# Performance work log

Hardware: AMD Instinct MI355X
Metric: run time of the kernel (lower is better)

Reference implementation:

```python
import jax, jax.numpy as jnp
import numpy as np

L = 4          # layers
HID = 64       # hidden channels per layer
CIN = 16       # patched input channels (1 * 4 * 4)
K = 5
PAD = 2
T_IN, T_OUT = 10, 10
FORGET_BIAS = 1.0
LN_EPS = 1e-5


def _conv(x, w, pad):
    return jax.lax.conv_general_dilated(
        x, w, window_strides=(1, 1), padding=[(pad, pad), (pad, pad)],
        dimension_numbers=('NCHW', 'OIHW', 'NCHW'))


def _ln(x):
    # LayerNorm over (C,H,W) per sample, no affine (gamma=1, beta=0)
    mu = jnp.mean(x, axis=(1, 2, 3), keepdims=True)
    var = jnp.var(x, axis=(1, 2, 3), keepdims=True)
    return (x - mu) * jax.lax.rsqrt(var + LN_EPS)


def _cell(x, h, c, m, Wx, Wh, Wm, Wo, Wl):
    # ST-LSTM cell (PredRNN V1) with layer norm on gate convs
    xcat = _ln(_conv(x, Wx, PAD))   # [B, 7*HID, H, W]
    hcat = _ln(_conv(h, Wh, PAD))   # [B, 4*HID, H, W]
    mcat = _ln(_conv(m, Wm, PAD))   # [B, 3*HID, H, W]
    ix, fx, gx, ixp, fxp, gxp, ox = jnp.split(xcat, 7, axis=1)
    ih, fh, gh, oh = jnp.split(hcat, 4, axis=1)
    im, fm, gm = jnp.split(mcat, 3, axis=1)
    i = jax.nn.sigmoid(ix + ih)
    f = jax.nn.sigmoid(fx + fh + FORGET_BIAS)
    g = jnp.tanh(gx + gh)
    c_new = f * c + i * g
    ip = jax.nn.sigmoid(ixp + im)
    fp = jax.nn.sigmoid(fxp + fm + FORGET_BIAS)
    gp = jnp.tanh(gxp + gm)
    m_new = fp * m + ip * gp
    mem = jnp.concatenate([c_new, m_new], axis=1)  # [B, 2*HID, H, W]
    o = jax.nn.sigmoid(ox + oh + _ln(_conv(mem, Wo, PAD)))
    h_new = o * jnp.tanh(_conv(mem, Wl, 0))        # conv_last is 1x1
    return h_new, c_new, m_new


def _run_layers(x_t, hs, cs, m, Wx0, Wxr, Wh, Wm, Wo, Wl):
    h_list, c_list = [], []
    h0, c0, m = _cell(x_t, hs[0], cs[0], m, Wx0, Wh[0], Wm[0], Wo[0], Wl[0])
    h_list.append(h0); c_list.append(c0)
    for i in range(1, L):
        hi, ci, m = _cell(h_list[-1], hs[i], cs[i], m,
                          Wxr[i - 1], Wh[i], Wm[i], Wo[i], Wl[i])
        h_list.append(hi); c_list.append(ci)
    return jnp.stack(h_list), jnp.stack(c_list), m


def setup_inputs() -> dict:
    key = jax.random.key(0)
    ks = jax.random.split(key, 9)
    s = 0.02
    return {
        'x_patched': jax.random.normal(ks[0], (4, T_IN + T_OUT, CIN, 32, 32), jnp.float32),
        'mask_patched': jax.random.uniform(ks[1], (4, T_IN + T_OUT - 2, 1, 32, 32), jnp.float32),
        'Wx0': jax.random.normal(ks[2], (7 * HID, CIN, K, K), jnp.float32) * s,
        'Wxr': jax.random.normal(ks[3], (L - 1, 7 * HID, HID, K, K), jnp.float32) * s,
        'Wh': jax.random.normal(ks[4], (L, 4 * HID, HID, K, K), jnp.float32) * s,
        'Wm': jax.random.normal(ks[5], (L, 3 * HID, HID, K, K), jnp.float32) * s,
        'Wo': jax.random.normal(ks[6], (L, HID, 2 * HID, K, K), jnp.float32) * s,
        'Wl': jax.random.normal(ks[7], (L, HID, 2 * HID, 1, 1), jnp.float32) * s,
        'Wout': jax.random.normal(ks[8], (CIN, HID, 1, 1), jnp.float32) * s,
    }


def reference(x_patched, mask_patched, Wx0, Wxr, Wh, Wm, Wo, Wl, Wout):
    B, T, _, H, W = x_patched.shape
    hs = jnp.zeros((L, B, HID, H, W), x_patched.dtype)
    cs = jnp.zeros((L, B, HID, H, W), x_patched.dtype)
    m = jnp.zeros((B, HID, H, W), x_patched.dtype)

    # t = 0: reverse scheduled sampling feeds ground truth
    hs, cs, m = _run_layers(x_patched[:, 0], hs, cs, m, Wx0, Wxr, Wh, Wm, Wo, Wl)
    x_out0 = _conv(hs[-1], Wout, 0)

    def scan_fn(carry, inp):
        hs, cs, m, x_out = carry
        x_frame, mask_t = inp
        x_t = mask_t * x_frame + (1.0 - mask_t) * x_out
        hs, cs, m = _run_layers(x_t, hs, cs, m, Wx0, Wxr, Wh, Wm, Wo, Wl)
        x_new = _conv(hs[-1], Wout, 0)
        return (hs, cs, m, x_new), x_new

    # t = 1 .. T-2: mask index t-1
    xs = (jnp.moveaxis(x_patched[:, 1:T - 1], 1, 0),
          jnp.moveaxis(mask_patched[:, :T - 2], 1, 0))
    _, outs = jax.lax.scan(scan_fn, (hs, cs, m, x_out0), xs)  # [T-2, B, CIN, H, W]
    x_next = jnp.concatenate([x_out0[:, None], jnp.moveaxis(outs, 0, 1)], axis=1)
    return x_next  # [B, T-1, CIN, H, W]; decouple_loss is identically 0 for V1
```

## Files before the change

kernel.cpp:

```cpp
#include <hip/hip_runtime.h>
#include <cstddef>
#include <cstdint>


#define BB 4
#define NLAYER 4
#define NSTEP 19

typedef _Float16 f16;
typedef _Float16 f16x8 __attribute__((ext_vector_type(8)));
typedef float f32x4 __attribute__((ext_vector_type(4)));

constexpr size_t OFF_HS    = 0;
constexpr size_t OFF_CS    = 1048576;
constexpr size_t OFF_M     = 2097152;
constexpr size_t OFF_STATS = 2359296;
constexpr size_t OFF_XRAW  = 2359360;
constexpr size_t OFF_HRAW  = 4194368;
constexpr size_t OFF_MRAW  = 5242944;
constexpr size_t OFF_MEM   = 6029376;
constexpr size_t OFF_OPART = 6553664;
constexpr size_t OFF_ORAW  = 7602240;
constexpr size_t OFF_OXH   = 7864384;
constexpr size_t OFF_WF    = 8126528;
constexpr size_t ZERO_N    = OFF_XRAW;

constexpr size_t WF_X0 = 0;
constexpr size_t WF_XR = 716800;
constexpr size_t WF_H  = 5017600;
constexpr size_t WF_M  = 8294400;
constexpr size_t WF_O  = 10752000;

__device__ __forceinline__ float sigmoidf_(float x) {
    return 1.0f / (1.0f + __expf(-x));
}

__device__ __forceinline__ float fast_tanh(float x) {
    float ax = fabsf(x);
    float e = __expf(2.0f * ax);
    float r = 1.0f - 2.0f / (e + 1.0f);
    return copysignf(r, x);
}

__device__ __forceinline__ void ln_params(const double* stats, int slot, int b,
                                          float N, float& mu, float& rs) {
    double s1 = stats[slot * 8 + b * 2 + 0];
    double s2 = stats[slot * 8 + b * 2 + 1];
    double mud = s1 / (double)N;
    double var = s2 / (double)N - mud * mud;
    mu = (float)mud;
    float v = (float)var + 1e-5f;
    float r = rsqrtf(v);
    r = r * (1.5f - 0.5f * v * r * r);
    rs = r;
}

__global__ __launch_bounds__(256)
void prep_k(const float* __restrict__ src, f16* __restrict__ dst,
            int CO, int CIs, int CIp) {
    int idx = blockIdx.x * 256 + threadIdx.x;
    int total = CO * CIp * 25;
    if (idx >= total) return;
    int ci = idx % CIp;
    int rem = idx / CIp;
    int co = rem % CO;
    int tap = rem / CO;
    float v = (ci < CIs) ? src[((size_t)co * CIs + ci) * 25 + tap] : 0.f;
    f16 hi = (f16)v;
    f16 lo = (f16)(v - (float)hi);
    dst[((size_t)(tap * 2 + 0) * CO + co) * CIp + ci] = hi;
    dst[((size_t)(tap * 2 + 1) * CO + co) * CIp + ci] = lo;
}

__global__ __launch_bounds__(256)
void mfconv_k(const float* __restrict__ xsrc, int xbstride, int xCI, int xCIpad,
              const f16* __restrict__ wfx,
              const float* __restrict__ hsrc, const f16* __restrict__ wfh,
              const float* __restrict__ msrc, const f16* __restrict__ wfm,
              const float* __restrict__ x_patched, const float* __restrict__ mask,
              const float* __restrict__ prevout, int t, int domix,
              float* __restrict__ xraw, float* __restrict__ hraw,
              float* __restrict__ mraw, double* __restrict__ stats) {
    __shared__ alignas(16) f16 lds[14208];
    const int tid = threadIdx.x;
    int bid = blockIdx.x;
    const int b = bid / 224;
    int g = bid % 224;
    int path, cog, pxg, CO, CI, CIpad;
    const f16* wf;
    const float* in;
    float* outp;
    if (g < 112) {
        path = 0; cog = g >> 4; pxg = g & 15;
        CO = 448; CI = xCI; CIpad = xCIpad; wf = wfx; outp = xraw;
        in = xsrc + (size_t)b * xbstride;
    } else if (g < 176) {
        g -= 112; path = 1; cog = g >> 4; pxg = g & 15;
        CO = 256; CI = 64; CIpad = 64; wf = wfh; outp = hraw;
        in = hsrc + (size_t)b * 65536;
    } else {
        g -= 176; path = 2; cog = g >> 4; pxg = g & 15;
        CO = 192; CI = 64; CIpad = 64; wf = wfm; outp = mraw;
        in = msrc + (size_t)b * 65536;
    }
    const int y0 = pxg * 2;
    const bool mix = (path == 0) && (domix != 0);

    const int ci_l = tid & 31, sr = tid >> 5;
    const int skg = ci_l >> 3, scb = ci_l & 7;
    const int sy = y0 - 2 + sr;
    const bool rowok = (sr < 6) && ((unsigned)sy < 32u);

    const int w = tid >> 6, lane = tid & 63;
    const int coh = w & 1, wr = w >> 1;
    const int n = lane & 15, kq = lane >> 4;
    const size_t wtap = (size_t)2 * CO * CIpad;
    const size_t laneA = (size_t)(cog * 64 + coh * 32 + n) * CIpad + kq * 8;
    const int pbase = (wr + 2) * 37 + 2 + n;

    f32x4 acc[2][2] = {};

    const int nchunks = CIpad >> 5;
    for (int chunk = 0; chunk < nchunks; ++chunk) {
        __syncthreads();
        {
            const int cig = chunk * 32 + ci_l;
            float v[32];
            #pragma unroll
            for (int k = 0; k < 32; ++k) v[k] = 0.f;
            if (rowok && cig < CI) {
                if (mix) {
                    const float* xfr = x_patched + ((size_t)b * 20 + t) * 16384
                                       + (size_t)cig * 1024 + sy * 32;
                    const float* xor_ = prevout
                                       + (((size_t)b * NSTEP + (t - 1)) * 16 + cig) * 1024
                                       + sy * 32;
                    const float* mkr = mask + ((size_t)b * 18 + (t - 1)) * 1024 + sy * 32;
                    #pragma unroll
                    for (int k = 0; k < 8; ++k) {
                        float4 a = *(const float4*)(xfr + k * 4);
                        float4 o = *(const float4*)(xor_ + k * 4);
                        float4 mm = *(const float4*)(mkr + k * 4);
                        v[4 * k + 0] = mm.x * a.x + (1.f - mm.x) * o.x;
                        v[4 * k + 1] = mm.y * a.y + (1.f - mm.y) * o.y;
                        v[4 * k + 2] = mm.z * a.z + (1.f - mm.z) * o.z;
                        v[4 * k + 3] = mm.w * a.w + (1.f - mm.w) * o.w;
                    }
                } else {
                    const float* rp = in + (size_t)cig * 1024 + sy * 32;
                    #pragma unroll
                    for (int k = 0; k < 8; ++k) {
                        float4 q = *(const float4*)(rp + k * 4);
                        v[4 * k + 0] = q.x; v[4 * k + 1] = q.y;
                        v[4 * k + 2] = q.z; v[4 * k + 3] = q.w;
                    }
                }
            }
            if (sr < 6) {
                #define STW(c, val) { int p = sr * 37 + (c);                         \
                    int s_ = skg ^ ((p >> 1) & 3);                                   \
                    int off = p * 32 + (s_ << 3) + scb;                              \
                    f16 hi = (f16)(val); f16 lo = (f16)((val) - (float)hi);          \
                    lds[off] = hi; lds[7104 + off] = lo; }
                STW(0, 0.f); STW(1, 0.f);
                #pragma unroll
                for (int x = 0; x < 32; ++x) STW(x + 2, v[x]);
                STW(34, 0.f); STW(35, 0.f);
                #undef STW
            }
        }
        __syncthreads();
        const f16* wfc = wf + chunk * 32;
        for (int ky = 0; ky < 5; ++ky) {
            const f16* wfk = wfc + (size_t)(ky * 5) * wtap;
            const int pky = pbase + (ky - 2) * 37;
            #pragma unroll
            for (int kx = 0; kx < 5; ++kx) {
                const f16* wA = wfk + (size_t)kx * wtap;
                const f16* wAl = wA + (size_t)CO * CIpad;
                f16x8 a0h = *(const f16x8*)(wA + laneA);
                f16x8 a1h = *(const f16x8*)(wA + laneA + (size_t)16 * CIpad);
                f16x8 a0l = *(const f16x8*)(wAl + laneA);
                f16x8 a1l = *(const f16x8*)(wAl + laneA + (size_t)16 * CIpad);
                #pragma unroll
                for (int pt = 0; pt < 2; ++pt) {
                    int p = pky + (kx - 2) + pt * 16;
                    int off = p * 32 + ((kq ^ ((p >> 1) & 3)) << 3);
                    f16x8 bh = *(const f16x8*)&lds[off];
                    f16x8 bl = *(const f16x8*)&lds[7104 + off];
                    acc[0][pt] = __builtin_amdgcn_mfma_f32_16x16x32_f16(a0h, bh, acc[0][pt], 0, 0, 0);
                    acc[1][pt] = __builtin_amdgcn_mfma_f32_16x16x32_f16(a1h, bh, acc[1][pt], 0, 0, 0);
                    acc[0][pt] = __builtin_amdgcn_mfma_f32_16x16x32_f16(a0l, bh, acc[0][pt], 0, 0, 0);
                    acc[1][pt] = __builtin_amdgcn_mfma_f32_16x16x32_f16(a1l, bh, acc[1][pt], 0, 0, 0);
                    acc[0][pt] = __builtin_amdgcn_mfma_f32_16x16x32_f16(a0h, bl, acc[0][pt], 0, 0, 0);
                    acc[1][pt] = __builtin_amdgcn_mfma_f32_16x16x32_f16(a1h, bl, acc[1][pt], 0, 0, 0);
                }
            }
        }
    }

    float* ob = outp + ((size_t)b * CO + cog * 64 + coh * 32) * 1024 + (y0 + wr) * 32;
    double s1 = 0.0, s2 = 0.0;
    #pragma unroll
    for (int ct = 0; ct < 2; ++ct)
        #pragma unroll
        for (int pt = 0; pt < 2; ++pt)
            #pragma unroll
            for (int j = 0; j < 4; ++j) {
                float vv = acc[ct][pt][j];
                ob[(size_t)(ct * 16 + kq * 4 + j) * 1024 + pt * 16 + n] = vv;
                s1 += vv; s2 += (double)vv * vv;
            }
    __syncthreads();
    double* red = (double*)lds;
    red[tid] = s1; red[256 + tid] = s2;
    __syncthreads();
    for (int s = 128; s > 0; s >>= 1) {
        if (tid < s) { red[tid] += red[tid + s]; red[256 + tid] += red[256 + tid + s]; }
        __syncthreads();
    }
    if (tid == 0) {
        atomicAdd(&stats[path * 8 + b * 2 + 0], red[0]);
        atomicAdd(&stats[path * 8 + b * 2 + 1], red[256]);
    }
}

__global__ __launch_bounds__(256)
void convo_mf_k(const float* __restrict__ mem, const f16* __restrict__ wfo,
                float* __restrict__ opart) {
    __shared__ alignas(16) f16 lds[14208];
    const int tid = threadIdx.x;
    const int bid = blockIdx.x;
    const int chunk = bid & 3;
    const int pxg = (bid >> 2) & 15;
    const int b = bid >> 6;
    const int y0 = pxg * 2;
    const float* in = mem + (size_t)b * 131072;

    const int ci_l = tid & 31, sr = tid >> 5;
    const int skg = ci_l >> 3, scb = ci_l & 7;
    const int sy = y0 - 2 + sr;
    const bool rowok = (sr < 6) && ((unsigned)sy < 32u);

    const int w = tid >> 6, lane = tid & 63;
    const int coh = w & 1, wr = w >> 1;
    const int n = lane & 15, kq = lane >> 4;
    const size_t wtap = (size_t)2 * 64 * 128;
    const size_t laneA = (size_t)(coh * 32 + n) * 128 + chunk * 32 + kq * 8;
    const int pbase = (wr + 2) * 37 + 2 + n;

    f32x4 acc[2][2] = {};

    {
        const int cig = chunk * 32 + ci_l;
        float v[32];
        #pragma unroll
        for (int k = 0; k < 32; ++k) v[k] = 0.f;
        if (rowok) {
            const float* rp = in + (size_t)cig * 1024 + sy * 32;
            #pragma unroll
            for (int k = 0; k < 8; ++k) {
                float4 q = *(const float4*)(rp + k * 4);
                v[4 * k + 0] = q.x; v[4 * k + 1] = q.y;
                v[4 * k + 2] = q.z; v[4 * k + 3] = q.w;
            }
        }
        if (sr < 6) {
            #define STW(c, val) { int p = sr * 37 + (c);                         \
                int s_ = skg ^ ((p >> 1) & 3);                                   \
                int off = p * 32 + (s_ << 3) + scb;                              \
                f16 hi = (f16)(val); f16 lo = (f16)((val) - (float)hi);          \
                lds[off] = hi; lds[7104 + off] = lo; }
            STW(0, 0.f); STW(1, 0.f);
            #pragma unroll
            for (int x = 0; x < 32; ++x) STW(x + 2, v[x]);
            STW(34, 0.f); STW(35, 0.f);
            #undef STW
        }
    }
    __syncthreads();
    for (int ky = 0; ky < 5; ++ky) {
        const f16* wfk = wfo + (size_t)(ky * 5) * wtap;
        const int pky = pbase + (ky - 2) * 37;
        #pragma unroll
        for (int kx = 0; kx < 5; ++kx) {
            const f16* wA = wfk + (size_t)kx * wtap;
            const f16* wAl = wA + (size_t)64 * 128;
            f16x8 a0h = *(const f16x8*)(wA + laneA);
            f16x8 a1h = *(const f16x8*)(wA + laneA + (size_t)16 * 128);
            f16x8 a0l = *(const f16x8*)(wAl + laneA);
            f16x8 a1l = *(const f16x8*)(wAl + laneA + (size_t)16 * 128);
            #pragma unroll
            for (int pt = 0; pt < 2; ++pt) {
                int p = pky + (kx - 2) + pt * 16;
                int off = p * 32 + ((kq ^ ((p >> 1) & 3)) << 3);
                f16x8 bh = *(const f16x8*)&lds[off];
                f16x8 bl = *(const f16x8*)&lds[7104 + off];
                acc[0][pt] = __builtin_amdgcn_mfma_f32_16x16x32_f16(a0h, bh, acc[0][pt], 0, 0, 0);
                acc[1][pt] = __builtin_amdgcn_mfma_f32_16x16x32_f16(a1h, bh, acc[1][pt], 0, 0, 0);
                acc[0][pt] = __builtin_amdgcn_mfma_f32_16x16x32_f16(a0l, bh, acc[0][pt], 0, 0, 0);
                acc[1][pt] = __builtin_amdgcn_mfma_f32_16x16x32_f16(a1l, bh, acc[1][pt], 0, 0, 0);
                acc[0][pt] = __builtin_amdgcn_mfma_f32_16x16x32_f16(a0h, bl, acc[0][pt], 0, 0, 0);
                acc[1][pt] = __builtin_amdgcn_mfma_f32_16x16x32_f16(a1h, bl, acc[1][pt], 0, 0, 0);
            }
        }
    }
    float* ob = opart + (size_t)chunk * 262144
              + ((size_t)b * 64 + coh * 32) * 1024 + (y0 + wr) * 32;
    #pragma unroll
    for (int ct = 0; ct < 2; ++ct)
        #pragma unroll
        for (int pt = 0; pt < 2; ++pt)
            #pragma unroll
            for (int j = 0; j < 4; ++j)
                ob[(size_t)(ct * 16 + kq * 4 + j) * 1024 + pt * 16 + n] = acc[ct][pt][j];
}

#define LD4(dst, p) { float4 _v = *reinterpret_cast<const float4*>(p); \
                      (dst)[0]=_v.x; (dst)[1]=_v.y; (dst)[2]=_v.z; (dst)[3]=_v.w; }
#define ST4(p, src) { *reinterpret_cast<float4*>(p) = \
                      make_float4((src)[0], (src)[1], (src)[2], (src)[3]); }

__global__ __launch_bounds__(256)
void gates_k(const float* __restrict__ xraw, const float* __restrict__ hraw,
             const float* __restrict__ mraw, double* __restrict__ stats,
             float* __restrict__ cs_l, float* __restrict__ m_buf,
             float* __restrict__ mem, float* __restrict__ oxh) {
    int e4 = blockIdx.x * 256 + threadIdx.x;
    if (e4 < 8) stats[24 + e4] = 0.0;
    int b = e4 >> 14;
    int r = (e4 & 16383) << 2;

    float mu_x, rs_x, mu_h, rs_h, mu_m, rs_m;
    ln_params(stats, 0, b, 458752.f, mu_x, rs_x);
    ln_params(stats, 1, b, 262144.f, mu_h, rs_h);
    ln_params(stats, 2, b, 196608.f, mu_m, rs_m);

    const float* xb = xraw + (size_t)b * 458752 + r;
    const float* hb = hraw + (size_t)b * 262144 + r;
    const float* mb = mraw + (size_t)b * 196608 + r;
    float* csb  = cs_l  + (size_t)b * 65536 + r;
    float* mbb  = m_buf + (size_t)b * 65536 + r;
    float* memc = mem   + (size_t)b * 131072 + r;
    float* memm = memc + 65536;
    float* oxb  = oxh   + (size_t)b * 65536 + r;

    float X[7][4], H[4][4], M[3][4], C[4], MM[4];
    #pragma unroll
    for (int k = 0; k < 7; ++k) LD4(X[k], xb + k * 65536);
    #pragma unroll
    for (int k = 0; k < 4; ++k) LD4(H[k], hb + k * 65536);
    #pragma unroll
    for (int k = 0; k < 3; ++k) LD4(M[k], mb + k * 65536);
    LD4(C, csb);
    LD4(MM, mbb);

    float cn[4], mn[4], ox4[4];
    #pragma unroll
    for (int j = 0; j < 4; ++j) {
        float ix  = (X[0][j] - mu_x) * rs_x;
        float fx  = (X[1][j] - mu_x) * rs_x;
        float gx  = (X[2][j] - mu_x) * rs_x;
        float ixp = (X[3][j] - mu_x) * rs_x;
        float fxp = (X[4][j] - mu_x) * rs_x;
        float gxp = (X[5][j] - mu_x) * rs_x;
        float ox  = (X[6][j] - mu_x) * rs_x;
        float ih  = (H[0][j] - mu_h) * rs_h;
        float fh  = (H[1][j] - mu_h) * rs_h;
        float gh  = (H[2][j] - mu_h) * rs_h;
        float oh  = (H[3][j] - mu_h) * rs_h;
        float im  = (M[0][j] - mu_m) * rs_m;
        float fm  = (M[1][j] - mu_m) * rs_m;
        float gm  = (M[2][j] - mu_m) * rs_m;

        float i  = sigmoidf_(ix + ih);
        float f  = sigmoidf_(fx + fh + 1.0f);
        float gg = fast_tanh(gx + gh);
        float c  = f * C[j] + i * gg;
        float ip = sigmoidf_(ixp + im);
        float fp = sigmoidf_(fxp + fm + 1.0f);
        float gp = fast_tanh(gxp + gm);
        float m2 = fp * MM[j] + ip * gp;
        cn[j] = c; mn[j] = m2; ox4[j] = ox + oh;
    }
    ST4(csb, cn); ST4(mbb, mn); ST4(memc, cn); ST4(memm, mn); ST4(oxb, ox4);
}

__global__ __launch_bounds__(256)
void statso_k(const float* __restrict__ opart, float* __restrict__ oraw,
              double* __restrict__ stats) {
    __shared__ double red[512];
    int e4 = blockIdx.x * 256 + threadIdx.x;
    int b = e4 >> 14;
    int r = e4 << 2;
    float4 v0 = *reinterpret_cast<const float4*>(opart + r);
    float4 v1 = *reinterpret_cast<const float4*>(opart + 262144 + r);
    float4 v2 = *reinterpret_cast<const float4*>(opart + 524288 + r);
    float4 v3 = *reinterpret_cast<const float4*>(opart + 786432 + r);
    float4 s;
    s.x = v0.x + v1.x + v2.x + v3.x;
    s.y = v0.y + v1.y + v2.y + v3.y;
    s.z = v0.z + v1.z + v2.z + v3.z;
    s.w = v0.w + v1.w + v2.w + v3.w;
    *reinterpret_cast<float4*>(oraw + r) = s;
    double s1 = (double)s.x + (double)s.y + (double)s.z + (double)s.w;
    double s2 = (double)s.x * s.x + (double)s.y * s.y +
                (double)s.z * s.z + (double)s.w * s.w;
    int t = threadIdx.x;
    red[t] = s1; red[256 + t] = s2;
    __syncthreads();
    for (int st = 128; st > 0; st >>= 1) {
        if (t < st) { red[t] += red[t + st]; red[256 + t] += red[256 + t + st]; }
        __syncthreads();
    }
    if (t == 0) {
        atomicAdd(&stats[24 + b * 2 + 0], red[0]);
        atomicAdd(&stats[24 + b * 2 + 1], red[256]);
    }
}

__global__ __launch_bounds__(256)
void final_k(const float* __restrict__ mem, const float* __restrict__ oraw,
             const float* __restrict__ oxh, double* __restrict__ stats,
             const float* __restrict__ Wl_l, float* __restrict__ hs_l) {
    int bi = blockIdx.x;
    int b = bi >> 4, pxq = (bi >> 2) & 3, coq = bi & 3;
    int px = pxq * 256 + threadIdx.x;
    const float* memb = mem + (size_t)b * 131072 + px;
    float acc[16];
    #pragma unroll
    for (int k = 0; k < 16; ++k) acc[k] = 0.f;
    for (int ci = 0; ci < 128; ++ci) {
        float v = memb[ci * 1024];
        #pragma unroll
        for (int k = 0; k < 16; ++k)
            acc[k] = fmaf(v, Wl_l[(coq * 16 + k) * 128 + ci], acc[k]);
    }
    float mu, rs;
    ln_params(stats, 3, b, 65536.f, mu, rs);
    #pragma unroll
    for (int k = 0; k < 16; ++k) {
        int co = coq * 16 + k;
        size_t idx = ((size_t)b * 64 + co) * 1024 + px;
        float o = sigmoidf_(oxh[idx] + (oraw[idx] - mu) * rs);
        hs_l[idx] = o * fast_tanh(acc[k]);
    }
    if (bi == 0 && threadIdx.x < 24) stats[threadIdx.x] = 0.0;
}

__global__ __launch_bounds__(256)
void out_k(const float* __restrict__ h3, const float* __restrict__ Wout,
           float* __restrict__ out, int t) {
    int e = blockIdx.x * 256 + threadIdx.x;
    int b = e >> 10, px = e & 1023;
    const float* hb = h3 + (size_t)b * 65536 + px;
    float acc[16];
    #pragma unroll
    for (int k = 0; k < 16; ++k) acc[k] = 0.f;
    for (int ci = 0; ci < 64; ++ci) {
        float v = hb[ci * 1024];
        #pragma unroll
        for (int k = 0; k < 16; ++k) acc[k] = fmaf(v, Wout[k * 64 + ci], acc[k]);
    }
    #pragma unroll
    for (int k = 0; k < 16; ++k)
        out[(((size_t)b * NSTEP + t) * 16 + k) * 1024 + px] = acc[k];
}

__global__ __launch_bounds__(256)
void init_k(float* __restrict__ ws) {
    size_t i = ((size_t)blockIdx.x * 256 + threadIdx.x) * 4;
    for (; i < ZERO_N; i += (size_t)gridDim.x * 1024)
        *reinterpret_cast<float4*>(ws + i) = make_float4(0.f, 0.f, 0.f, 0.f);
}

extern "C" void kernel_launch(void* const* d_in, const int* in_sizes, int n_in,
                              void* d_out, int out_size, void* d_ws, size_t ws_size,
                              hipStream_t stream) {
    const float* x_patched = (const float*)d_in[0];
    const float* mask      = (const float*)d_in[1];
    const float* Wx0       = (const float*)d_in[2];
    const float* Wxr       = (const float*)d_in[3];
    const float* Wh        = (const float*)d_in[4];
    const float* Wm        = (const float*)d_in[5];
    const float* Wo        = (const float*)d_in[6];
    const float* Wl        = (const float*)d_in[7];
    const float* Wout      = (const float*)d_in[8];
    float* out = (float*)d_out;
    float* ws  = (float*)d_ws;

    float* hs    = ws + OFF_HS;
    float* cs    = ws + OFF_CS;
    float* m_buf = ws + OFF_M;
    double* stats = (double*)(ws + OFF_STATS);
    float* xraw  = ws + OFF_XRAW;
    float* hraw  = ws + OFF_HRAW;
    float* mraw  = ws + OFF_MRAW;
    float* mem   = ws + OFF_MEM;
    float* opart = ws + OFF_OPART;
    float* oraw  = ws + OFF_ORAW;
    float* oxh   = ws + OFF_OXH;
    f16*   wfb   = (f16*)(ws + OFF_WF);

    init_k<<<1024, 256, 0, stream>>>(ws);

    prep_k<<<(448 * 32 * 25 + 255) / 256, 256, 0, stream>>>(
        Wx0, wfb + WF_X0, 448, 16, 32);
    for (int lr = 0; lr < 3; ++lr)
        prep_k<<<(448 * 64 * 25 + 255) / 256, 256, 0, stream>>>(
            Wxr + (size_t)lr * 448 * 64 * 25, wfb + WF_XR + (size_t)lr * 1433600,
            448, 64, 64);
    for (int l = 0; l < 4; ++l)
        prep_k<<<(256 * 64 * 25 + 255) / 256, 256, 0, stream>>>(
            Wh + (size_t)l * 256 * 64 * 25, wfb + WF_H + (size_t)l * 819200,
            256, 64, 64);
    for (int l = 0; l < 4; ++l)
        prep_k<<<(192 * 64 * 25 + 255) / 256, 256, 0, stream>>>(
            Wm + (size_t)l * 192 * 64 * 25, wfb + WF_M + (size_t)l * 614400,
            192, 64, 64);
    for (int l = 0; l < 4; ++l)
        prep_k<<<(64 * 128 * 25 + 255) / 256, 256, 0, stream>>>(
            Wo + (size_t)l * 64 * 128 * 25, wfb + WF_O + (size_t)l * 409600,
            64, 128, 128);

    for (int t = 0; t < NSTEP; ++t) {
        for (int l = 0; l < NLAYER; ++l) {
            const float* xsrc;
            int xbstride, domix, xCI, xCIpad;
            const f16* wfx;
            if (l == 0) {
                xsrc = x_patched; xCI = 16; xCIpad = 32; wfx = wfb + WF_X0;
                if (t == 0) { xbstride = 327680; domix = 0; }
                else        { xbstride = 0;      domix = 1; }
            } else {
                xsrc = hs + (size_t)(l - 1) * 262144;
                xbstride = 65536; domix = 0; xCI = 64; xCIpad = 64;
                wfx = wfb + WF_XR + (size_t)(l - 1) * 1433600;
            }
            mfconv_k<<<dim3(BB * 224), 256, 0, stream>>>(
                xsrc, xbstride, xCI, xCIpad, wfx,
                hs + (size_t)l * 262144, wfb + WF_H + (size_t)l * 819200,
                m_buf, wfb + WF_M + (size_t)l * 614400,
                x_patched, mask, out, t, domix,
                xraw, hraw, mraw, stats);
            gates_k<<<256, 256, 0, stream>>>(
                xraw, hraw, mraw, stats,
                cs + (size_t)l * 262144, m_buf, mem, oxh);
            convo_mf_k<<<dim3(256), 256, 0, stream>>>(
                mem, wfb + WF_O + (size_t)l * 409600, opart);
            statso_k<<<256, 256, 0, stream>>>(opart, oraw, stats);
            final_k<<<64, 256, 0, stream>>>(
                mem, oraw, oxh, stats,
                Wl + (size_t)l * 64 * 128, hs + (size_t)l * 262144);
        }
        out_k<<<16, 256, 0, stream>>>(hs + 3 * 262144, Wout, out, t);
    }
    (void)in_sizes; (void)n_in; (void)out_size; (void)ws_size;
}
```

Baseline: 13.47 ms.

## Fuse all per-step kernels into one persistent kernel with software grid barriers

Replaces the roughly 400 separate kernel launches (weight prep, conv, gates, conv_o, stats, final, output) with a single persistent kernel of 256 blocks that loops over timesteps and layers and uses an atomic-counter grid barrier between phases. The goal is to remove per-launch overhead and inter-kernel gaps on a latency-bound recurrent workload. The main conv phase now runs 896 work units over 256 blocks, so per-phase parallelism drops compared with the 896-block launches. The separate partial-sum buffer for conv_o is removed, and the persistent design depends on all 256 blocks being co-resident to avoid deadlock.

```diff
diff --git a/kernel.cpp b/kernel.cpp
--- a/kernel.cpp
+++ b/kernel.cpp
@@ -3,9 +3,9 @@
 #include <cstdint>
 
 
-#define BB 4
 #define NLAYER 4
 #define NSTEP 19
+#define GRID 256
 
 typedef _Float16 f16;
 typedef _Float16 f16x8 __attribute__((ext_vector_type(8)));
@@ -19,10 +19,10 @@
 constexpr size_t OFF_HRAW  = 4194368;
 constexpr size_t OFF_MRAW  = 5242944;
 constexpr size_t OFF_MEM   = 6029376;
-constexpr size_t OFF_OPART = 6553664;
-constexpr size_t OFF_ORAW  = 7602240;
-constexpr size_t OFF_OXH   = 7864384;
-constexpr size_t OFF_WF    = 8126528;
+constexpr size_t OFF_ORAW  = 6553664;
+constexpr size_t OFF_OXH   = 6815808;
+constexpr size_t OFF_WF    = 7077952;
+constexpr size_t OFF_BAR   = 13273152;
 constexpr size_t ZERO_N    = OFF_XRAW;
 
 constexpr size_t WF_X0 = 0;
@@ -30,6 +30,19 @@
 constexpr size_t WF_H  = 5017600;
 constexpr size_t WF_M  = 8294400;
 constexpr size_t WF_O  = 10752000;
+
+struct P {
+    const float* x_patched; const float* mask;
+    const float* Wx0; const float* Wxr; const float* Wh;
+    const float* Wm; const float* Wo; const float* Wl; const float* Wout;
+    float* out;
+    float* hs; float* cs; float* m_buf;
+    double* stats;
+    float* xraw; float* hraw; float* mraw;
+    float* mem; float* oraw; float* oxh;
+    f16* wfx0; f16* wfxr; f16* wfh; f16* wfm; f16* wfo;
+    unsigned* bar; unsigned* gen;
+};
 
 __device__ __forceinline__ float sigmoidf_(float x) {
     return 1.0f / (1.0f + __expf(-x));
@@ -55,56 +68,73 @@
     rs = r;
 }
 
-__global__ __launch_bounds__(256)
-void prep_k(const float* __restrict__ src, f16* __restrict__ dst,
-            int CO, int CIs, int CIp) {
-    int idx = blockIdx.x * 256 + threadIdx.x;
+__device__ __forceinline__ void gridbar(unsigned* bar, unsigned* gen) {
+    __syncthreads();
+    if (threadIdx.x == 0) {
+        __threadfence();
+        unsigned g = __hip_atomic_load(gen, __ATOMIC_RELAXED, __HIP_MEMORY_SCOPE_AGENT);
+        unsigned v = __hip_atomic_fetch_add(bar, 1u, __ATOMIC_ACQ_REL, __HIP_MEMORY_SCOPE_AGENT);
+        if (v == (unsigned)GRID - 1u) {
+            __hip_atomic_store(bar, 0u, __ATOMIC_RELAXED, __HIP_MEMORY_SCOPE_AGENT);
+            __hip_atomic_fetch_add(gen, 1u, __ATOMIC_RELEASE, __HIP_MEMORY_SCOPE_AGENT);
+        } else {
+            while (__hip_atomic_load(gen, __ATOMIC_ACQUIRE, __HIP_MEMORY_SCOPE_AGENT) == g)
+                __builtin_amdgcn_s_sleep(8);
+        }
+        __threadfence();
+    }
+    __syncthreads();
+}
+
+__device__ void prep_dev(const float* __restrict__ src, f16* __restrict__ dst,
+                         int CO, int CIs, int CIp, int gid, int gs) {
     int total = CO * CIp * 25;
-    if (idx >= total) return;
-    int ci = idx % CIp;
-    int rem = idx / CIp;
-    int co = rem % CO;
-    int tap = rem / CO;
-    float v = (ci < CIs) ? src[((size_t)co * CIs + ci) * 25 + tap] : 0.f;
-    f16 hi = (f16)v;
-    f16 lo = (f16)(v - (float)hi);
-    dst[((size_t)(tap * 2 + 0) * CO + co) * CIp + ci] = hi;
-    dst[((size_t)(tap * 2 + 1) * CO + co) * CIp + ci] = lo;
-}
-
-__global__ __launch_bounds__(256)
-void mfconv_k(const float* __restrict__ xsrc, int xbstride, int xCI, int xCIpad,
-              const f16* __restrict__ wfx,
-              const float* __restrict__ hsrc, const f16* __restrict__ wfh,
-              const float* __restrict__ msrc, const f16* __restrict__ wfm,
-              const float* __restrict__ x_patched, const float* __restrict__ mask,
-              const float* __restrict__ prevout, int t, int domix,
-              float* __restrict__ xraw, float* __restrict__ hraw,
-              float* __restrict__ mraw, double* __restrict__ stats) {
-    __shared__ alignas(16) f16 lds[14208];
+    for (int idx = gid; idx < total; idx += gs) {
+        int ci = idx % CIp;
+        int rem = idx / CIp;
+        int co = rem % CO;
+        int tap = rem / CO;
+        float v = (ci < CIs) ? src[((size_t)co * CIs + ci) * 25 + tap] : 0.f;
+        f16 hi = (f16)v;
+        f16 lo = (f16)(v - (float)hi);
+        dst[((size_t)(tap * 2 + 0) * CO + co) * CIp + ci] = hi;
+        dst[((size_t)(tap * 2 + 1) * CO + co) * CIp + ci] = lo;
+    }
+}
+
+__device__ __forceinline__ void phaseA(const P& p, f16* lds, int t, int l, int u) {
     const int tid = threadIdx.x;
-    int bid = blockIdx.x;
-    const int b = bid / 224;
-    int g = bid % 224;
+    const int b = u / 224;
+    int g = u - b * 224;
     int path, cog, pxg, CO, CI, CIpad;
     const f16* wf;
     const float* in;
     float* outp;
     if (g < 112) {
-        path = 0; cog = g >> 4; pxg = g & 15;
-        CO = 448; CI = xCI; CIpad = xCIpad; wf = wfx; outp = xraw;
-        in = xsrc + (size_t)b * xbstride;
+        path = 0; cog = g >> 4; pxg = g & 15; CO = 448;
+        if (l == 0) {
+            CI = 16; CIpad = 32; wf = p.wfx0;
+            in = p.x_patched + (size_t)b * 327680;
+        } else {
+            CI = 64; CIpad = 64; wf = p.wfxr + (size_t)(l - 1) * 1433600;
+            in = p.hs + (size_t)(l - 1) * 262144 + (size_t)b * 65536;
+        }
+        outp = p.xraw;
     } else if (g < 176) {
-        g -= 112; path = 1; cog = g >> 4; pxg = g & 15;
-        CO = 256; CI = 64; CIpad = 64; wf = wfh; outp = hraw;
-        in = hsrc + (size_t)b * 65536;
+        int gg = g - 112;
+        path = 1; cog = gg >> 4; pxg = gg & 15; CO = 256; CI = 64; CIpad = 64;
+        wf = p.wfh + (size_t)l * 819200;
+        in = p.hs + (size_t)l * 262144 + (size_t)b * 65536;
+        outp = p.hraw;
     } else {
-        g -= 176; path = 2; cog = g >> 4; pxg = g & 15;
-        CO = 192; CI = 64; CIpad = 64; wf = wfm; outp = mraw;
-        in = msrc + (size_t)b * 65536;
+        int gg = g - 176;
+        path = 2; cog = gg >> 4; pxg = gg & 15; CO = 192; CI = 64; CIpad = 64;
+        wf = p.wfm + (size_t)l * 614400;
+        in = p.m_buf + (size_t)b * 65536;
+        outp = p.mraw;
     }
     const int y0 = pxg * 2;
-    const bool mix = (path == 0) && (domix != 0);
+    const bool mix = (path == 0) && (l == 0) && (t > 0);
 
     const int ci_l = tid & 31, sr = tid >> 5;
     const int skg = ci_l >> 3, scb = ci_l & 7;
@@ -115,7 +145,7 @@
     const int coh = w & 1, wr = w >> 1;
     const int n = lane & 15, kq = lane >> 4;
     const size_t wtap = (size_t)2 * CO * CIpad;
-    const size_t laneA = (size_t)(cog * 64 + coh * 32 + n) * CIpad + kq * 8;
+    const size_t laneA0 = (size_t)(cog * 64 + coh * 32 + n) * CIpad + kq * 8;
     const int pbase = (wr + 2) * 37 + 2 + n;
 
     f32x4 acc[2][2] = {};
@@ -130,16 +160,16 @@
             for (int k = 0; k < 32; ++k) v[k] = 0.f;
             if (rowok && cig < CI) {
                 if (mix) {
-                    const float* xfr = x_patched + ((size_t)b * 20 + t) * 16384
+                    const float* xfr = p.x_patched + ((size_t)b * 20 + t) * 16384
                                        + (size_t)cig * 1024 + sy * 32;
-                    const float* xor_ = prevout
+                    const float* xop = p.out
                                        + (((size_t)b * NSTEP + (t - 1)) * 16 + cig) * 1024
                                        + sy * 32;
-                    const float* mkr = mask + ((size_t)b * 18 + (t - 1)) * 1024 + sy * 32;
+                    const float* mkr = p.mask + ((size_t)b * 18 + (t - 1)) * 1024 + sy * 32;
                     #pragma unroll
                     for (int k = 0; k < 8; ++k) {
                         float4 a = *(const float4*)(xfr + k * 4);
-                        float4 o = *(const float4*)(xor_ + k * 4);
+                        float4 o = *(const float4*)(xop + k * 4);
                         float4 mm = *(const float4*)(mkr + k * 4);
                         v[4 * k + 0] = mm.x * a.x + (1.f - mm.x) * o.x;
                         v[4 * k + 1] = mm.y * a.y + (1.f - mm.y) * o.y;
@@ -157,9 +187,9 @@
                 }
             }
             if (sr < 6) {
-                #define STW(c, val) { int p = sr * 37 + (c);                         \
-                    int s_ = skg ^ ((p >> 1) & 3);                                   \
-                    int off = p * 32 + (s_ << 3) + scb;                              \
+                #define STW(c, val) { int pp = sr * 37 + (c);                        \
+                    int s_ = skg ^ ((pp >> 1) & 3);                                  \
+                    int off = pp * 32 + (s_ << 3) + scb;                             \
                     f16 hi = (f16)(val); f16 lo = (f16)((val) - (float)hi);          \
                     lds[off] = hi; lds[7104 + off] = lo; }
                 STW(0, 0.f); STW(1, 0.f);
@@ -178,14 +208,14 @@
             for (int kx = 0; kx < 5; ++kx) {
                 const f16* wA = wfk + (size_t)kx * wtap;
                 const f16* wAl = wA + (size_t)CO * CIpad;
-                f16x8 a0h = *(const f16x8*)(wA + laneA);
-                f16x8 a1h = *(const f16x8*)(wA + laneA + (size_t)16 * CIpad);
-                f16x8 a0l = *(const f16x8*)(wAl + laneA);
-                f16x8 a1l = *(const f16x8*)(wAl + laneA + (size_t)16 * CIpad);
+                f16x8 a0h = *(const f16x8*)(wA + laneA0);
+                f16x8 a1h = *(const f16x8*)(wA + laneA0 + (size_t)16 * CIpad);
+                f16x8 a0l = *(const f16x8*)(wAl + laneA0);
+                f16x8 a1l = *(const f16x8*)(wAl + laneA0 + (size_t)16 * CIpad);
                 #pragma unroll
                 for (int pt = 0; pt < 2; ++pt) {
-                    int p = pky + (kx - 2) + pt * 16;
-                    int off = p * 32 + ((kq ^ ((p >> 1) & 3)) << 3);
+                    int pp = pky + (kx - 2) + pt * 16;
+                    int off = pp * 32 + ((kq ^ ((pp >> 1) & 3)) << 3);
                     f16x8 bh = *(const f16x8*)&lds[off];
                     f16x8 bl = *(const f16x8*)&lds[7104 + off];
                     acc[0][pt] = __builtin_amdgcn_mfma_f32_16x16x32_f16(a0h, bh, acc[0][pt], 0, 0, 0);
@@ -220,130 +250,37 @@
         __syncthreads();
     }
     if (tid == 0) {
-        atomicAdd(&stats[path * 8 + b * 2 + 0], red[0]);
-        atomicAdd(&stats[path * 8 + b * 2 + 1], red[256]);
-    }
-}
-
-__global__ __launch_bounds__(256)
-void convo_mf_k(const float* __restrict__ mem, const f16* __restrict__ wfo,
-                float* __restrict__ opart) {
-    __shared__ alignas(16) f16 lds[14208];
-    const int tid = threadIdx.x;
-    const int bid = blockIdx.x;
-    const int chunk = bid & 3;
-    const int pxg = (bid >> 2) & 15;
-    const int b = bid >> 6;
-    const int y0 = pxg * 2;
-    const float* in = mem + (size_t)b * 131072;
-
-    const int ci_l = tid & 31, sr = tid >> 5;
-    const int skg = ci_l >> 3, scb = ci_l & 7;
-    const int sy = y0 - 2 + sr;
-    const bool rowok = (sr < 6) && ((unsigned)sy < 32u);
-
-    const int w = tid >> 6, lane = tid & 63;
-    const int coh = w & 1, wr = w >> 1;
-    const int n = lane & 15, kq = lane >> 4;
-    const size_t wtap = (size_t)2 * 64 * 128;
-    const size_t laneA = (size_t)(coh * 32 + n) * 128 + chunk * 32 + kq * 8;
-    const int pbase = (wr + 2) * 37 + 2 + n;
-
-    f32x4 acc[2][2] = {};
-
-    {
-        const int cig = chunk * 32 + ci_l;
-        float v[32];
-        #pragma unroll
-        for (int k = 0; k < 32; ++k) v[k] = 0.f;
-        if (rowok) {
-            const float* rp = in + (size_t)cig * 1024 + sy * 32;
-            #pragma unroll
-            for (int k = 0; k < 8; ++k) {
-                float4 q = *(const float4*)(rp + k * 4);
-                v[4 * k + 0] = q.x; v[4 * k + 1] = q.y;
-                v[4 * k + 2] = q.z; v[4 * k + 3] = q.w;
-            }
-        }
-        if (sr < 6) {
-            #define STW(c, val) { int p = sr * 37 + (c);                         \
-                int s_ = skg ^ ((p >> 1) & 3);                                   \
-                int off = p * 32 + (s_ << 3) + scb;                              \
-                f16 hi = (f16)(val); f16 lo = (f16)((val) - (float)hi);          \
-                lds[off] = hi; lds[7104 + off] = lo; }
-            STW(0, 0.f); STW(1, 0.f);
-            #pragma unroll
-            for (int x = 0; x < 32; ++x) STW(x + 2, v[x]);
-            STW(34, 0.f); STW(35, 0.f);
-            #undef STW
-        }
-    }
-    __syncthreads();
-    for (int ky = 0; ky < 5; ++ky) {
-        const f16* wfk = wfo + (size_t)(ky * 5) * wtap;
-        const int pky = pbase + (ky - 2) * 37;
-        #pragma unroll
-        for (int kx = 0; kx < 5; ++kx) {
-            const f16* wA = wfk + (size_t)kx * wtap;
-            const f16* wAl = wA + (size_t)64 * 128;
-            f16x8 a0h = *(const f16x8*)(wA + laneA);
-            f16x8 a1h = *(const f16x8*)(wA + laneA + (size_t)16 * 128);
-            f16x8 a0l = *(const f16x8*)(wAl + laneA);
-            f16x8 a1l = *(const f16x8*)(wAl + laneA + (size_t)16 * 128);
-            #pragma unroll
-            for (int pt = 0; pt < 2; ++pt) {
-                int p = pky + (kx - 2) + pt * 16;
-                int off = p * 32 + ((kq ^ ((p >> 1) & 3)) << 3);
-                f16x8 bh = *(const f16x8*)&lds[off];
-                f16x8 bl = *(const f16x8*)&lds[7104 + off];
-                acc[0][pt] = __builtin_amdgcn_mfma_f32_16x16x32_f16(a0h, bh, acc[0][pt], 0, 0, 0);
-                acc[1][pt] = __builtin_amdgcn_mfma_f32_16x16x32_f16(a1h, bh, acc[1][pt], 0, 0, 0);
-                acc[0][pt] = __builtin_amdgcn_mfma_f32_16x16x32_f16(a0l, bh, acc[0][pt], 0, 0, 0);
-                acc[1][pt] = __builtin_amdgcn_mfma_f32_16x16x32_f16(a1l, bh, acc[1][pt], 0, 0, 0);
-                acc[0][pt] = __builtin_amdgcn_mfma_f32_16x16x32_f16(a0h, bl, acc[0][pt], 0, 0, 0);
-                acc[1][pt] = __builtin_amdgcn_mfma_f32_16x16x32_f16(a1h, bl, acc[1][pt], 0, 0, 0);
-            }
-        }
-    }
-    float* ob = opart + (size_t)chunk * 262144
-              + ((size_t)b * 64 + coh * 32) * 1024 + (y0 + wr) * 32;
-    #pragma unroll
-    for (int ct = 0; ct < 2; ++ct)
-        #pragma unroll
-        for (int pt = 0; pt < 2; ++pt)
-            #pragma unroll
-            for (int j = 0; j < 4; ++j)
-                ob[(size_t)(ct * 16 + kq * 4 + j) * 1024 + pt * 16 + n] = acc[ct][pt][j];
-}
-
-#define LD4(dst, p) { float4 _v = *reinterpret_cast<const float4*>(p); \
-                      (dst)[0]=_v.x; (dst)[1]=_v.y; (dst)[2]=_v.z; (dst)[3]=_v.w; }
-#define ST4(p, src) { *reinterpret_cast<float4*>(p) = \
-                      make_float4((src)[0], (src)[1], (src)[2], (src)[3]); }
-
-__global__ __launch_bounds__(256)
-void gates_k(const float* __restrict__ xraw, const float* __restrict__ hraw,
-             const float* __restrict__ mraw, double* __restrict__ stats,
-             float* __restrict__ cs_l, float* __restrict__ m_buf,
-             float* __restrict__ mem, float* __restrict__ oxh) {
+        atomicAdd(&p.stats[path * 8 + b * 2 + 0], red[0]);
+        atomicAdd(&p.stats[path * 8 + b * 2 + 1], red[256]);
+    }
+    __syncthreads();
+}
+
+#define LD4(dst, ptr) { float4 _v = *reinterpret_cast<const float4*>(ptr); \
+                        (dst)[0]=_v.x; (dst)[1]=_v.y; (dst)[2]=_v.z; (dst)[3]=_v.w; }
+#define ST4(ptr, src) { *reinterpret_cast<float4*>(ptr) = \
+                        make_float4((src)[0], (src)[1], (src)[2], (src)[3]); }
+
+__device__ __forceinline__ void phaseB(const P& p, int l) {
     int e4 = blockIdx.x * 256 + threadIdx.x;
-    if (e4 < 8) stats[24 + e4] = 0.0;
+    if (e4 >= 65536) return;
+    if (e4 < 8) p.stats[24 + e4] = 0.0;
     int b = e4 >> 14;
     int r = (e4 & 16383) << 2;
 
     float mu_x, rs_x, mu_h, rs_h, mu_m, rs_m;
-    ln_params(stats, 0, b, 458752.f, mu_x, rs_x);
-    ln_params(stats, 1, b, 262144.f, mu_h, rs_h);
-    ln_params(stats, 2, b, 196608.f, mu_m, rs_m);
-
-    const float* xb = xraw + (size_t)b * 458752 + r;
-    const float* hb = hraw + (size_t)b * 262144 + r;
-    const float* mb = mraw + (size_t)b * 196608 + r;
-    float* csb  = cs_l  + (size_t)b * 65536 + r;
-    float* mbb  = m_buf + (size_t)b * 65536 + r;
-    float* memc = mem   + (size_t)b * 131072 + r;
+    ln_params(p.stats, 0, b, 458752.f, mu_x, rs_x);
+    ln_params(p.stats, 1, b, 262144.f, mu_h, rs_h);
+    ln_params(p.stats, 2, b, 196608.f, mu_m, rs_m);
+
+    const float* xb = p.xraw + (size_t)b * 458752 + r;
+    const float* hb = p.hraw + (size_t)b * 262144 + r;
+    const float* mb = p.mraw + (size_t)b * 196608 + r;
+    float* csb  = p.cs + (size_t)l * 262144 + (size_t)b * 65536 + r;
+    float* mbb  = p.m_buf + (size_t)b * 65536 + r;
+    float* memc = p.mem + (size_t)b * 131072 + r;
     float* memm = memc + 65536;
-    float* oxb  = oxh   + (size_t)b * 65536 + r;
+    float* oxb  = p.oxh + (size_t)b * 65536 + r;
 
     float X[7][4], H[4][4], M[3][4], C[4], MM[4];
     #pragma unroll
@@ -386,174 +323,236 @@
     ST4(csb, cn); ST4(mbb, mn); ST4(memc, cn); ST4(memm, mn); ST4(oxb, ox4);
 }
 
-__global__ __launch_bounds__(256)
-void statso_k(const float* __restrict__ opart, float* __restrict__ oraw,
-              double* __restrict__ stats) {
-    __shared__ double red[512];
-    int e4 = blockIdx.x * 256 + threadIdx.x;
-    int b = e4 >> 14;
-    int r = e4 << 2;
-    float4 v0 = *reinterpret_cast<const float4*>(opart + r);
-    float4 v1 = *reinterpret_cast<const float4*>(opart + 262144 + r);
-    float4 v2 = *reinterpret_cast<const float4*>(opart + 524288 + r);
-    float4 v3 = *reinterpret_cast<const float4*>(opart + 786432 + r);
-    float4 s;
-    s.x = v0.x + v1.x + v2.x + v3.x;
-    s.y = v0.y + v1.y + v2.y + v3.y;
-    s.z = v0.z + v1.z + v2.z + v3.z;
-    s.w = v0.w + v1.w + v2.w + v3.w;
-    *reinterpret_cast<float4*>(oraw + r) = s;
-    double s1 = (double)s.x + (double)s.y + (double)s.z + (double)s.w;
-    double s2 = (double)s.x * s.x + (double)s.y * s.y +
-                (double)s.z * s.z + (double)s.w * s.w;
-    int t = threadIdx.x;
-    red[t] = s1; red[256 + t] = s2;
-    __syncthreads();
-    for (int st = 128; st > 0; st >>= 1) {
-        if (t < st) { red[t] += red[t + st]; red[256 + t] += red[256 + t + st]; }
+__device__ __forceinline__ void phaseC(const P& p, f16* lds, int l) {
+    const int bid = blockIdx.x;
+    const int tid = threadIdx.x;
+    if (bid >= 128) {
+        if (bid == 128 && tid < 24) p.stats[tid] = 0.0;
+        return;
+    }
+    const int b = bid >> 5;
+    const int pxg = (bid >> 1) & 15;
+    const int coh = bid & 1;
+    const int y0 = pxg * 2;
+    const float* in = p.mem + (size_t)b * 131072;
+    const f16* wfo = p.wfo + (size_t)l * 409600;
+
+    const int ci_l = tid & 31, sr = tid >> 5;
+    const int skg = ci_l >> 3, scb = ci_l & 7;
+    const int sy = y0 - 2 + sr;
+    const bool rowok = (sr < 6) && ((unsigned)sy < 32u);
+
+    const int w = tid >> 6, lane = tid & 63;
+    const int coq = w & 1, wr = w >> 1;
+    const int n = lane & 15, kq = lane >> 4;
+    const size_t wtap = (size_t)2 * 64 * 128;
+    const int pbase = (wr + 2) * 37 + 2 + n;
+
+    f32x4 acc[2] = {};
+
+    for (int chunk = 0; chunk < 4; ++chunk) {
         __syncthreads();
-    }
-    if (t == 0) {
-        atomicAdd(&stats[24 + b * 2 + 0], red[0]);
-        atomicAdd(&stats[24 + b * 2 + 1], red[256]);
-    }
-}
-
-__global__ __launch_bounds__(256)
-void final_k(const float* __restrict__ mem, const float* __restrict__ oraw,
-             const float* __restrict__ oxh, double* __restrict__ stats,
-             const float* __restrict__ Wl_l, float* __restrict__ hs_l) {
-    int bi = blockIdx.x;
-    int b = bi >> 4, pxq = (bi >> 2) & 3, coq = bi & 3;
-    int px = pxq * 256 + threadIdx.x;
-    const float* memb = mem + (size_t)b * 131072 + px;
-    float acc[16];
-    #pragma unroll
-    for (int k = 0; k < 16; ++k) acc[k] = 0.f;
+        {
+            const int cig = chunk * 32 + ci_l;
+            float v[32];
+            #pragma unroll
+            for (int k = 0; k < 32; ++k) v[k] = 0.f;
+            if (rowok) {
+                const float* rp = in + (size_t)cig * 1024 + sy * 32;
+                #pragma unroll
+                for (int k = 0; k < 8; ++k) {
+                    float4 q = *(const float4*)(rp + k * 4);
+                    v[4 * k + 0] = q.x; v[4 * k + 1] = q.y;
+                    v[4 * k + 2] = q.z; v[4 * k + 3] = q.w;
+                }
+            }
+            if (sr < 6) {
+                #define STW(c, val) { int pp = sr * 37 + (c);                        \
+                    int s_ = skg ^ ((pp >> 1) & 3);                                  \
+                    int off = pp * 32 + (s_ << 3) + scb;                             \
+                    f16 hi = (f16)(val); f16 lo = (f16)((val) - (float)hi);          \
+                    lds[off] = hi; lds[7104 + off] = lo; }
+                STW(0, 0.f); STW(1, 0.f);
+                #pragma unroll
+                for (int x = 0; x < 32; ++x) STW(x + 2, v[x]);
+                STW(34, 0.f); STW(35, 0.f);
+                #undef STW
+            }
+        }
+        __syncthreads();
+        const size_t laneA = (size_t)(coh * 32 + coq * 16 + n) * 128 + chunk * 32 + kq * 8;
+        for (int ky = 0; ky < 5; ++ky) {
+            const f16* wfk = wfo + (size_t)(ky * 5) * wtap;
+            const int pky = pbase + (ky - 2) * 37;
+            #pragma unroll
+            for (int kx = 0; kx < 5; ++kx) {
+                const f16* wA = wfk + (size_t)kx * wtap;
+                f16x8 ah = *(const f16x8*)(wA + laneA);
+                f16x8 al = *(const f16x8*)(wA + (size_t)64 * 128 + laneA);
+                #pragma unroll
+                for (int pt = 0; pt < 2; ++pt) {
+                    int pp = pky + (kx - 2) + pt * 16;
+                    int off = pp * 32 + ((kq ^ ((pp >> 1) & 3)) << 3);
+                    f16x8 bh = *(const f16x8*)&lds[off];
+                    f16x8 bl = *(const f16x8*)&lds[7104 + off];
+                    acc[pt] = __builtin_amdgcn_mfma_f32_16x16x32_f16(ah, bh, acc[pt], 0, 0, 0);
+                    acc[pt] = __builtin_amdgcn_mfma_f32_16x16x32_f16(al, bh, acc[pt], 0, 0, 0);
+                    acc[pt] = __builtin_amdgcn_mfma_f32_16x16x32_f16(ah, bl, acc[pt], 0, 0, 0);
+                }
+            }
+        }
+    }
+
+    float* ob = p.oraw + ((size_t)b * 64 + coh * 32 + coq * 16) * 1024 + (y0 + wr) * 32;
+    double s1 = 0.0, s2 = 0.0;
+    #pragma unroll
+    for (int pt = 0; pt < 2; ++pt)
+        #pragma unroll
+        for (int j = 0; j < 4; ++j) {
+            float vv = acc[pt][j];
+            ob[(size_t)(kq * 4 + j) * 1024 + pt * 16 + n] = vv;
+            s1 += vv; s2 += (double)vv * vv;
+        }
+    __syncthreads();
+    double* red = (double*)lds;
+    red[tid] = s1; red[256 + tid] = s2;
+    __syncthreads();
+    for (int s = 128; s > 0; s >>= 1) {
+        if (tid < s) { red[tid] += red[tid + s]; red[256 + tid] += red[256 + tid + s]; }
+        __syncthreads();
+    }
+    if (tid == 0) {
+        atomicAdd(&p.stats[24 + b * 2 + 0], red[0]);
+        atomicAdd(&p.stats[24 + b * 2 + 1], red[256]);
+    }
+}
+
+__device__ __forceinline__ void phaseD(const P& p, int l) {
+    const int bid = blockIdx.x;
+    if (bid >= 256) return;
+    const int tid = threadIdx.x;
+    const int b = bid >> 6;
+    const int pxq = (bid >> 2) & 15;
+    const int coq = bid & 3;
+    const int px = pxq * 64 + (tid & 63);
+    const int co0 = coq * 16 + (tid >> 6) * 4;
+    const float* memb = p.mem + (size_t)b * 131072 + px;
+    const float* Wl_l = p.Wl + (size_t)l * 8192;
+    float acc[4] = {0.f, 0.f, 0.f, 0.f};
     for (int ci = 0; ci < 128; ++ci) {
         float v = memb[ci * 1024];
         #pragma unroll
-        for (int k = 0; k < 16; ++k)
-            acc[k] = fmaf(v, Wl_l[(coq * 16 + k) * 128 + ci], acc[k]);
+        for (int k = 0; k < 4; ++k)
+            acc[k] = fmaf(v, Wl_l[(co0 + k) * 128 + ci], acc[k]);
     }
     float mu, rs;
-    ln_params(stats, 3, b, 65536.f, mu, rs);
-    #pragma unroll
-    for (int k = 0; k < 16; ++k) {
-        int co = coq * 16 + k;
-        size_t idx = ((size_t)b * 64 + co) * 1024 + px;
-        float o = sigmoidf_(oxh[idx] + (oraw[idx] - mu) * rs);
+    ln_params(p.stats, 3, b, 65536.f, mu, rs);
+    float* hs_l = p.hs + (size_t)l * 262144;
+    #pragma unroll
+    for (int k = 0; k < 4; ++k) {
+        size_t idx = ((size_t)b * 64 + co0 + k) * 1024 + px;
+        float o = sigmoidf_(p.oxh[idx] + (p.oraw[idx] - mu) * rs);
         hs_l[idx] = o * fast_tanh(acc[k]);
     }
-    if (bi == 0 && threadIdx.x < 24) stats[threadIdx.x] = 0.0;
-}
-
-__global__ __launch_bounds__(256)
-void out_k(const float* __restrict__ h3, const float* __restrict__ Wout,
-           float* __restrict__ out, int t) {
-    int e = blockIdx.x * 256 + threadIdx.x;
-    int b = e >> 10, px = e & 1023;
-    const float* hb = h3 + (size_t)b * 65536 + px;
+}
+
+__device__ __forceinline__ void phaseOUT(const P& p, int t) {
+    int gid = blockIdx.x * 256 + threadIdx.x;
+    if (gid >= 4096) return;
+    int b = gid >> 10, px = gid & 1023;
+    const float* hb = p.hs + (size_t)3 * 262144 + (size_t)b * 65536 + px;
     float acc[16];
     #pragma unroll
     for (int k = 0; k < 16; ++k) acc[k] = 0.f;
     for (int ci = 0; ci < 64; ++ci) {
         float v = hb[ci * 1024];
         #pragma unroll
-        for (int k = 0; k < 16; ++k) acc[k] = fmaf(v, Wout[k * 64 + ci], acc[k]);
+        for (int k = 0; k < 16; ++k) acc[k] = fmaf(v, p.Wout[k * 64 + ci], acc[k]);
     }
     #pragma unroll
     for (int k = 0; k < 16; ++k)
-        out[(((size_t)b * NSTEP + t) * 16 + k) * 1024 + px] = acc[k];
-}
-
-__global__ __launch_bounds__(256)
-void init_k(float* __restrict__ ws) {
-    size_t i = ((size_t)blockIdx.x * 256 + threadIdx.x) * 4;
-    for (; i < ZERO_N; i += (size_t)gridDim.x * 1024)
-        *reinterpret_cast<float4*>(ws + i) = make_float4(0.f, 0.f, 0.f, 0.f);
+        p.out[(((size_t)b * NSTEP + t) * 16 + k) * 1024 + px] = acc[k];
+}
+
+__global__ __launch_bounds__(256, 2)
+void mega_k(P p) {
+    __shared__ alignas(16) f16 lds[14208];
+
+    {
+        const int gid = blockIdx.x * 256 + threadIdx.x;
+        const int gs = GRID * 256;
+        float4 z = make_float4(0.f, 0.f, 0.f, 0.f);
+        for (size_t i = (size_t)gid * 4; i < ZERO_N; i += (size_t)gs * 4)
+            *reinterpret_cast<float4*>(p.hs + i) = z;
+        prep_dev(p.Wx0, p.wfx0, 448, 16, 32, gid, gs);
+        for (int lr = 0; lr < 3; ++lr)
+            prep_dev(p.Wxr + (size_t)lr * 716800, p.wfxr + (size_t)lr * 1433600,
+                     448, 64, 64, gid, gs);
+        for (int l = 0; l < 4; ++l) {
+            prep_dev(p.Wh + (size_t)l * 409600, p.wfh + (size_t)l * 819200,
+                     256, 64, 64, gid, gs);
+            prep_dev(p.Wm + (size_t)l * 307200, p.wfm + (size_t)l * 614400,
+                     192, 64, 64, gid, gs);
+            prep_dev(p.Wo + (size_t)l * 204800, p.wfo + (size_t)l * 409600,
+                     64, 128, 128, gid, gs);
+        }
+    }
+    gridbar(p.bar, p.gen);
+
+    for (int t = 0; t < NSTEP; ++t) {
+        for (int l = 0; l < NLAYER; ++l) {
+            for (int u = blockIdx.x; u < 896; u += GRID)
+                phaseA(p, lds, t, l, u);
+            gridbar(p.bar, p.gen);
+            phaseB(p, l);
+            gridbar(p.bar, p.gen);
+            phaseC(p, lds, l);
+            gridbar(p.bar, p.gen);
+            phaseD(p, l);
+            gridbar(p.bar, p.gen);
+        }
+        phaseOUT(p, t);
+        gridbar(p.bar, p.gen);
+    }
 }
 
 extern "C" void kernel_launch(void* const* d_in, const int* in_sizes, int n_in,
                               void* d_out, int out_size, void* d_ws, size_t ws_size,
                               hipStream_t stream) {
-    const float* x_patched = (const float*)d_in[0];
-    const float* mask      = (const float*)d_in[1];
-    const float* Wx0       = (const float*)d_in[2];
-    const float* Wxr       = (const float*)d_in[3];
-    const float* Wh        = (const float*)d_in[4];
-    const float* Wm        = (const float*)d_in[5];
-    const float* Wo        = (const float*)d_in[6];
-    const float* Wl        = (const float*)d_in[7];
-    const float* Wout      = (const float*)d_in[8];
-    float* out = (float*)d_out;
-    float* ws  = (float*)d_ws;
-
-    float* hs    = ws + OFF_HS;
-    float* cs    = ws + OFF_CS;
-    float* m_buf = ws + OFF_M;
-    double* stats = (double*)(ws + OFF_STATS);
-    float* xraw  = ws + OFF_XRAW;
-    float* hraw  = ws + OFF_HRAW;
-    float* mraw  = ws + OFF_MRAW;
-    float* mem   = ws + OFF_MEM;
-    float* opart = ws + OFF_OPART;
-    float* oraw  = ws + OFF_ORAW;
-    float* oxh   = ws + OFF_OXH;
-    f16*   wfb   = (f16*)(ws + OFF_WF);
-
-    init_k<<<1024, 256, 0, stream>>>(ws);
-
-    prep_k<<<(448 * 32 * 25 + 255) / 256, 256, 0, stream>>>(
-        Wx0, wfb + WF_X0, 448, 16, 32);
-    for (int lr = 0; lr < 3; ++lr)
-        prep_k<<<(448 * 64 * 25 + 255) / 256, 256, 0, stream>>>(
-            Wxr + (size_t)lr * 448 * 64 * 25, wfb + WF_XR + (size_t)lr * 1433600,
-            448, 64, 64);
-    for (int l = 0; l < 4; ++l)
-        prep_k<<<(256 * 64 * 25 + 255) / 256, 256, 0, stream>>>(
-            Wh + (size_t)l * 256 * 64 * 25, wfb + WF_H + (size_t)l * 819200,
-            256, 64, 64);
-    for (int l = 0; l < 4; ++l)
-        prep_k<<<(192 * 64 * 25 + 255) / 256, 256, 0, stream>>>(
-            Wm + (size_t)l * 192 * 64 * 25, wfb + WF_M + (size_t)l * 614400,
-            192, 64, 64);
-    for (int l = 0; l < 4; ++l)
-        prep_k<<<(64 * 128 * 25 + 255) / 256, 256, 0, stream>>>(
-            Wo + (size_t)l * 64 * 128 * 25, wfb + WF_O + (size_t)l * 409600,
-            64, 128, 128);
-
-    for (int t = 0; t < NSTEP; ++t) {
-        for (int l = 0; l < NLAYER; ++l) {
-            const float* xsrc;
-            int xbstride, domix, xCI, xCIpad;
-            const f16* wfx;
-            if (l == 0) {
-                xsrc = x_patched; xCI = 16; xCIpad = 32; wfx = wfb + WF_X0;
-                if (t == 0) { xbstride = 327680; domix = 0; }
-                else        { xbstride = 0;      domix = 1; }
-            } else {
-                xsrc = hs + (size_t)(l - 1) * 262144;
-                xbstride = 65536; domix = 0; xCI = 64; xCIpad = 64;
-                wfx = wfb + WF_XR + (size_t)(l - 1) * 1433600;
-            }
-            mfconv_k<<<dim3(BB * 224), 256, 0, stream>>>(
-                xsrc, xbstride, xCI, xCIpad, wfx,
-                hs + (size_t)l * 262144, wfb + WF_H + (size_t)l * 819200,
-                m_buf, wfb + WF_M + (size_t)l * 614400,
-                x_patched, mask, out, t, domix,
-                xraw, hraw, mraw, stats);
-            gates_k<<<256, 256, 0, stream>>>(
-                xraw, hraw, mraw, stats,
-                cs + (size_t)l * 262144, m_buf, mem, oxh);
-            convo_mf_k<<<dim3(256), 256, 0, stream>>>(
-                mem, wfb + WF_O + (size_t)l * 409600, opart);
-            statso_k<<<256, 256, 0, stream>>>(opart, oraw, stats);
-            final_k<<<64, 256, 0, stream>>>(
-                mem, oraw, oxh, stats,
-                Wl + (size_t)l * 64 * 128, hs + (size_t)l * 262144);
-        }
-        out_k<<<16, 256, 0, stream>>>(hs + 3 * 262144, Wout, out, t);
-    }
+    float* ws = (float*)d_ws;
+    P pv;
+    pv.x_patched = (const float*)d_in[0];
+    pv.mask      = (const float*)d_in[1];
+    pv.Wx0       = (const float*)d_in[2];
+    pv.Wxr       = (const float*)d_in[3];
+    pv.Wh        = (const float*)d_in[4];
+    pv.Wm        = (const float*)d_in[5];
+    pv.Wo        = (const float*)d_in[6];
+    pv.Wl        = (const float*)d_in[7];
+    pv.Wout      = (const float*)d_in[8];
+    pv.out   = (float*)d_out;
+    pv.hs    = ws + OFF_HS;
+    pv.cs    = ws + OFF_CS;
+    pv.m_buf = ws + OFF_M;
+    pv.stats = (double*)(ws + OFF_STATS);
+    pv.xraw  = ws + OFF_XRAW;
+    pv.hraw  = ws + OFF_HRAW;
+    pv.mraw  = ws + OFF_MRAW;
+    pv.mem   = ws + OFF_MEM;
+    pv.oraw  = ws + OFF_ORAW;
+    pv.oxh   = ws + OFF_OXH;
+    f16* wfb = (f16*)(ws + OFF_WF);
+    pv.wfx0 = wfb + WF_X0;
+    pv.wfxr = wfb + WF_XR;
+    pv.wfh  = wfb + WF_H;
+    pv.wfm  = wfb + WF_M;
+    pv.wfo  = wfb + WF_O;
+    pv.bar  = (unsigned*)(ws + OFF_BAR);
+    pv.gen  = pv.bar + 1;
+
+    hipMemsetAsync((void*)pv.bar, 0, 2 * sizeof(unsigned), stream);
+
+    mega_k<<<dim3(GRID), dim3(256), 0, stream>>>(pv);
+
     (void)in_sizes; (void)n_in; (void)out_size; (void)ws_size;
 }
```

Result: slower. 42.79 ms (+217.7%).
